# Performance work log

Measured on AMD Instinct MI355X. Metric: run time of the kernel, lower is better.

Reference implementation:

```python
import jax, jax.numpy as jnp
import numpy as np

H, W, D = 56, 56, 28            # input_resolution
WS = (7, 7, 7)                  # window size (Wh, Ww, Wd)
SS = (3, 3, 3)                  # shift size
DIM = 96
NH = 3
HD = DIM // NH
N = WS[0] * WS[1] * WS[2]       # 343 tokens per window
NW = (H // WS[0]) * (W // WS[1]) * (D // WS[2])  # 256 windows


def _rel_pos_index():
    Wd, Wh, Ww = WS
    coords = np.stack(np.meshgrid(np.arange(Wd), np.arange(Wh), np.arange(Ww), indexing='ij'))
    cf = coords.reshape(3, -1)
    rel = (cf[:, :, None] - cf[:, None, :]).transpose(1, 2, 0)
    rel[:, :, 0] += Wd - 1
    rel[:, :, 1] += Wh - 1
    rel[:, :, 2] += Ww - 1
    rel[:, :, 0] *= (2 * Wh - 1) * (2 * Ww - 1)
    rel[:, :, 1] *= (2 * Ww - 1)
    return rel.sum(-1)  # (N, N)


def _attn_mask():
    img = np.zeros((H, W, D), np.float32)
    def slices(w, s):
        return (slice(0, -w), slice(-w, -s), slice(-s, None))
    cnt = 0
    for hs in slices(WS[0], SS[0]):
        for ws in slices(WS[1], SS[1]):
            for ds in slices(WS[2], SS[2]):
                img[hs, ws, ds] = cnt
                cnt += 1
    mw = img.reshape(H // WS[0], WS[0], W // WS[1], WS[1], D // WS[2], WS[2])
    mw = mw.transpose(0, 2, 4, 1, 3, 5).reshape(-1, N)  # (NW, N)
    am = mw[:, None, :] - mw[:, :, None]
    return np.where(am != 0, np.float32(-100.0), np.float32(0.0))


REL_IDX = jnp.asarray(_rel_pos_index())
ATTN_MASK = jnp.asarray(_attn_mask())  # (NW, N, N)


def _ln(x, g, b, eps=1e-5):
    m = x.mean(-1, keepdims=True)
    v = jnp.mean((x - m) ** 2, -1, keepdims=True)
    return (x - m) * jax.lax.rsqrt(v + eps) * g + b


def _forward(x, n1g, n1b, qkv_w, qkv_b, rpb, proj_w, proj_b,
             n2g, n2b, fc1_w, fc1_b, fc2_w, fc2_b):
    B, L, C = x.shape
    shortcut = x
    h = _ln(x, n1g, n1b).reshape(B, H, W, D, C)
    # cyclic shift
    h = jnp.roll(h, (-SS[0], -SS[1], -SS[2]), axis=(1, 2, 3))
    # window partition -> (B*NW, N, C)
    h = h.reshape(B, H // WS[0], WS[0], W // WS[1], WS[1], D // WS[2], WS[2], C)
    h = h.transpose(0, 1, 3, 5, 2, 4, 6, 7).reshape(-1, N, C)
    # qkv
    qkv = (h @ qkv_w + qkv_b).reshape(-1, N, 3, NH, HD).transpose(2, 0, 3, 1, 4)
    q, k, v = qkv[0] * (HD ** -0.5), qkv[1], qkv[2]  # (B*NW, NH, N, HD)
    attn = jnp.einsum('bhnd,bhmd->bhnm', q, k)
    bias = rpb[REL_IDX.reshape(-1)].reshape(N, N, NH).transpose(2, 0, 1)
    attn = attn + bias[None]
    # shifted-window mask
    attn = attn.reshape(B, NW, NH, N, N) + ATTN_MASK[None, :, None]
    attn = jax.nn.softmax(attn.reshape(-1, NH, N, N), axis=-1)
    o = jnp.einsum('bhnm,bhmd->bhnd', attn, v).transpose(0, 2, 1, 3).reshape(-1, N, C)
    o = o @ proj_w + proj_b
    # window reverse
    o = o.reshape(B, H // WS[0], W // WS[1], D // WS[2], WS[0], WS[1], WS[2], C)
    o = o.transpose(0, 1, 4, 2, 5, 3, 6, 7).reshape(B, H, W, D, C)
    o = jnp.roll(o, SS, axis=(1, 2, 3)).reshape(B, L, C)
    x = shortcut + o
    h2 = _ln(x, n2g, n2b)
    h2 = jax.nn.gelu(h2 @ fc1_w + fc1_b, approximate=False) @ fc2_w + fc2_b
    return x + h2


def setup_inputs() -> dict:
    key = jax.random.key(0)
    ks = jax.random.split(key, 6)
    C, FF = DIM, 4 * DIM
    f32 = jnp.float32
    return {
        'x': jax.random.normal(ks[0], (1, H * W * D, C), f32),
        'n1g': jnp.ones((C,), f32), 'n1b': jnp.zeros((C,), f32),
        'qkv_w': jax.random.normal(ks[1], (C, 3 * C), f32) * 0.02,
        'qkv_b': jnp.zeros((3 * C,), f32),
        'rpb': jax.random.normal(ks[2], ((2 * WS[0] - 1) * (2 * WS[1] - 1) * (2 * WS[2] - 1), NH), f32) * 0.02,
        'proj_w': jax.random.normal(ks[3], (C, C), f32) * 0.02,
        'proj_b': jnp.zeros((C,), f32),
        'n2g': jnp.ones((C,), f32), 'n2b': jnp.zeros((C,), f32),
        'fc1_w': jax.random.normal(ks[4], (C, FF), f32) * 0.02,
        'fc1_b': jnp.zeros((FF,), f32),
        'fc2_w': jax.random.normal(ks[5], (FF, C), f32) * 0.02,
        'fc2_b': jnp.zeros((C,), f32),
    }


def reference(x, n1g, n1b, qkv_w, qkv_b, rpb, proj_w, proj_b,
              n2g, n2b, fc1_w, fc1_b, fc2_w, fc2_b):
    return _forward(x, n1g, n1b, qkv_w, qkv_b, rpb, proj_w, proj_b,
                    n2g, n2b, fc1_w, fc1_b, fc2_w, fc2_b)
```

## Files before the change

kernel.cpp:

```cpp
#include <hip/hip_runtime.h>
#include <hip/hip_bf16.h>


#define L_TOK 87808

typedef unsigned int uint;
typedef __attribute__((ext_vector_type(8))) short short8;
typedef __attribute__((ext_vector_type(4))) float f32x4;

__device__ __forceinline__ float bflo(uint u){ union{uint x; float f;} a; a.x = u << 16; return a.f; }
__device__ __forceinline__ float bfhi(uint u){ union{uint x; float f;} a; a.x = u & 0xffff0000u; return a.f; }
__device__ __forceinline__ float bfval(unsigned short w){ union{uint x; float f;} a; a.x = (uint)w << 16; return a.f; }
__device__ __forceinline__ unsigned short f2bfbits(float f){
  union{float f; uint u;} a; a.f = f;
  uint u = a.u;
  u += 0x7fffu + ((u >> 16) & 1u);
  return (unsigned short)(u >> 16);
}
__device__ __forceinline__ unsigned short bfb(float f){
  __hip_bfloat16 h = __float2bfloat16(f);
  return *reinterpret_cast<unsigned short*>(&h);
}
__device__ __forceinline__ uint pkbf(float a, float b){
  return ((uint)bfb(b) << 16) | (uint)bfb(a);
}
__device__ __forceinline__ uint pack2(float a, float b){
  return ((uint)f2bfbits(b) << 16) | (uint)f2bfbits(a);
}
__device__ __forceinline__ uint4 pack8(const float* p){
  uint4 u;
  u.x = pack2(p[0], p[1]); u.y = pack2(p[2], p[3]);
  u.z = pack2(p[4], p[5]); u.w = pack2(p[6], p[7]);
  return u;
}
__device__ __forceinline__ uint4 pack8g(const float* gp){
  float t[8];
  *(float4*)&t[0] = *(const float4*)gp;
  *(float4*)&t[4] = *(const float4*)(gp + 4);
  return pack8(t);
}
__device__ __forceinline__ float gelu_f(float v){
  const float ax = fabsf(v) * 0.70710678118654752f;
  const float t  = 1.0f / (1.0f + 0.3275911f * ax);
  const float poly = t*(0.254829592f + t*(-0.284496736f + t*(1.421413741f +
                     t*(-1.453152027f + t*1.061405429f))));
  float erfv = 1.0f - poly * __expf(-ax*ax);
  erfv = copysignf(erfv, v);
  return 0.5f * v * (1.0f + erfv);
}

__global__ __launch_bounds__(256)
void k_tr(const float* __restrict__ src, unsigned short* __restrict__ dst,
          int K, int N)
{
  const int idx = blockIdx.x * 256 + threadIdx.x;
  if (idx < K * N) {
    const int n = idx / K, k = idx % K;
    dst[idx] = f2bfbits(src[(size_t)k * N + n]);
  }
}

__global__ __launch_bounds__(256)
void k_mb(const float* __restrict__ rpbg, unsigned short* __restrict__ MB)
{
  const int idx = blockIdx.x * 256 + threadIdx.x;
  const int cls = idx / (3*352*352);
  const int rem = idx - cls * (3*352*352);
  const int h = rem / (352*352);
  const int rem2 = rem - h * (352*352);
  const int q = rem2 / 352;
  const int k = rem2 - q * 352;
  unsigned short v = 0xFF80;
  if (q < 343 && k < 343) {
    const int q0 = q/49, q1 = (q%49)/7, q2 = q%7;
    const int k0 = k/49, k1 = (k%49)/7, k2 = k%7;
    const int bq = q0*169 + q1*13 + q2;
    const int bk = k0*169 + k1*13 + k2;
    float bias = rpbg[(size_t)(bq - bk + 1098)*3 + h];
    int cq = 0, ck = 0;
    if (cls & 4) { cq += ((q0 < 4) ? 1 : 2)*9; ck += ((k0 < 4) ? 1 : 2)*9; }
    if (cls & 2) { cq += ((q1 < 4) ? 1 : 2)*3; ck += ((k1 < 4) ? 1 : 2)*3; }
    if (cls & 1) { cq += (q2 < 4) ? 1 : 2;     ck += (k2 < 4) ? 1 : 2; }
    if (cq != ck) bias -= 100.0f;
    v = f2bfbits(bias);
  }
  MB[idx] = v;
}

__global__ __launch_bounds__(256)
void k_qkv_ln(const float* __restrict__ x,
              const float* __restrict__ n1g,
              const float* __restrict__ n1b,
              const unsigned short* __restrict__ qkvwt,
              const float* __restrict__ bias, size_t headStride,
              __hip_bfloat16* __restrict__ qb,
              __hip_bfloat16* __restrict__ kb,
              __hip_bfloat16* __restrict__ vb)
{
  __shared__ __align__(16) unsigned short As[64][104];
  __shared__ uint srcOff[64];
  __shared__ float gLds[96], bLds[96];
  __shared__ float pSum[256], pSq[256];
  __shared__ float mLds[64], sLds[64];

  const int tid = threadIdx.x;
  const int wave = tid >> 6, lane = tid & 63;
  const int row0 = blockIdx.x * 64;

  if (tid < 64) {
    const uint row = (uint)(row0 + tid);
    const uint win = row / 343u, n = row % 343u;
    const uint wh = win >> 5, ww = (win >> 2) & 7u, wd = win & 3u;
    const uint ih = n / 49u, rr = n % 49u, iw = rr / 7u, id = rr % 7u;
    uint gh = wh*7u + ih + 3u; if (gh >= 56u) gh -= 56u;
    uint gw = ww*7u + iw + 3u; if (gw >= 56u) gw -= 56u;
    uint gd = wd*7u + id + 3u; if (gd >= 28u) gd -= 28u;
    srcOff[tid] = ((gh*56u + gw)*28u + gd) * 96u;
  }
  if (tid < 96) { gLds[tid] = n1g[tid]; bLds[tid] = n1b[tid]; }
  __syncthreads();

  for (int i = tid; i < 768; i += 256) {
    const int r = i / 12, kk = (i % 12) * 8;
    *(uint4*)&As[r][kk] = pack8g(x + srcOff[r] + kk);
  }
  __syncthreads();

  {
    const int r = tid & 63, seg = tid >> 6;
    float s = 0.0f, sq = 0.0f;
    #pragma unroll
    for (int j3 = 0; j3 < 3; ++j3) {
      const uint4 u = *(const uint4*)&As[r][seg*24 + j3*8];
      float v[8];
      v[0]=bflo(u.x); v[1]=bfhi(u.x); v[2]=bflo(u.y); v[3]=bfhi(u.y);
      v[4]=bflo(u.z); v[5]=bfhi(u.z); v[6]=bflo(u.w); v[7]=bfhi(u.w);
      #pragma unroll
      for (int j = 0; j < 8; ++j) { s += v[j]; sq += v[j]*v[j]; }
    }
    pSum[tid] = s; pSq[tid] = sq;
  }
  __syncthreads();
  if (tid < 64) {
    const float s  = pSum[tid] + pSum[tid+64] + pSum[tid+128] + pSum[tid+192];
    const float sq = pSq[tid] + pSq[tid+64] + pSq[tid+128] + pSq[tid+192];
    const float mean = s * (1.0f/96.0f);
    mLds[tid] = mean;
    sLds[tid] = rsqrtf(sq*(1.0f/96.0f) - mean*mean + 1e-5f);
  }
  __syncthreads();
  for (int i = tid; i < 768; i += 256) {
    const int r = i / 12, kk = (i % 12) * 8;
    uint4 u = *(uint4*)&As[r][kk];
    const float m = mLds[r], sc = sLds[r];
    float v[8];
    v[0]=bflo(u.x); v[1]=bfhi(u.x); v[2]=bflo(u.y); v[3]=bfhi(u.y);
    v[4]=bflo(u.z); v[5]=bfhi(u.z); v[6]=bflo(u.w); v[7]=bfhi(u.w);
    #pragma unroll
    for (int j = 0; j < 8; ++j) v[j] = (v[j] - m)*sc*gLds[kk+j] + bLds[kk+j];
    *(uint4*)&As[r][kk] = pack8(v);
  }
  __syncthreads();

  f32x4 acc[18];
  #pragma unroll
  for (int i = 0; i < 18; ++i) acc[i] = (f32x4){0.f, 0.f, 0.f, 0.f};
  const int ml = lane & 15, q8 = (lane >> 4) * 8;
  #pragma unroll
  for (int kc = 0; kc < 3; ++kc) {
    const short8 a = *(const short8*)&As[wave*16 + ml][kc*32 + q8];
    #pragma unroll
    for (int nt = 0; nt < 18; ++nt) {
      const short8 b = *(const short8*)(qkvwt + (size_t)(nt*16 + ml)*96 + kc*32 + q8);
      acc[nt] = __builtin_amdgcn_mfma_f32_16x16x32_bf16(a, b, acc[nt], 0, 0, 0);
    }
  }

  const float qscale = 0.17677669529663687f;
  #pragma unroll
  for (int nt = 0; nt < 18; ++nt) {
    const int nbase = nt * 16;
    const int part = nbase / 96;
    const int rem  = nbase - part * 96;
    const int h    = rem >> 5;
    const int dbase= rem & 31;
    __hip_bfloat16* base = (part == 0) ? qb : ((part == 1) ? kb : vb);
    __hip_bfloat16* dst = base + (size_t)h * headStride;
    const float bv = bias[nbase + ml];
    #pragma unroll
    for (int r = 0; r < 4; ++r) {
      const size_t row = (size_t)(row0 + wave*16 + (lane >> 4)*4 + r);
      float v = acc[nt][r] + bv;
      if (part == 0) v *= qscale;
      dst[row*32 + dbase + ml] = __float2bfloat16(v);
    }
  }
}

__global__ __launch_bounds__(256, 4)
void k_attn_v10(const __hip_bfloat16* __restrict__ qg,
                const __hip_bfloat16* __restrict__ kg,
                const __hip_bfloat16* __restrict__ vg,
                size_t headStride,
                const unsigned short* __restrict__ MB,
                float* __restrict__ ob)
{
  __shared__ __align__(16) unsigned short vt[32*344 + 16];
  __shared__ __align__(16) unsigned short Pc[4][16*56];
  __shared__ float lred[4][16];

  const int tid = threadIdx.x;
  const int wave = tid >> 6, lane = tid & 63;
  const uint win = blockIdx.x;
  const int hh = (int)blockIdx.y;
  const int mtBase = (int)blockIdx.z * 11;
  const size_t wbase = (size_t)hh * headStride + (size_t)win * (343*32);
  const unsigned short* qw = (const unsigned short*)qg + wbase;
  const unsigned short* kw = (const unsigned short*)kg + wbase;
  const unsigned short* vw = (const unsigned short*)vg + wbase;

  const uint wh = win >> 5, ww = (win >> 2) & 7u, wd = win & 3u;
  const int cls = ((wh == 7u) ? 4 : 0) | ((ww == 7u) ? 2 : 0) | ((wd == 3u) ? 1 : 0);
  const unsigned short* MBh = MB + ((size_t)cls*3 + hh) * (352*352);

  for (int t = tid; t < 343; t += 256) {
    const uint4* src = (const uint4*)(vw + (size_t)t*32);
    #pragma unroll
    for (int c4 = 0; c4 < 4; ++c4) {
      const uint4 u = src[c4];
      const int d = c4*8;
      vt[(d+0)*344 + t] = (unsigned short)(u.x & 0xffffu);
      vt[(d+1)*344 + t] = (unsigned short)(u.x >> 16);
      vt[(d+2)*344 + t] = (unsigned short)(u.y & 0xffffu);
      vt[(d+3)*344 + t] = (unsigned short)(u.y >> 16);
      vt[(d+4)*344 + t] = (unsigned short)(u.z & 0xffffu);
      vt[(d+5)*344 + t] = (unsigned short)(u.z >> 16);
      vt[(d+6)*344 + t] = (unsigned short)(u.w & 0xffffu);
      vt[(d+7)*344 + t] = (unsigned short)(u.w >> 16);
    }
  }
  if (tid < 32) vt[tid*344 + 343] = 0;
  if (tid < 16) vt[32*344 + tid] = 0;
  __syncthreads();

  const int ml = lane & 15, g = lane >> 4, g8 = g*8;
  unsigned short* Pw = &Pc[wave][0];

  for (int mt = mtBase + wave; mt < mtBase + 11; mt += 4) {
    const int q = mt*16 + ml;
    const short8 qf = *(const short8*)(qw + (size_t)q*32 + g8);
    const unsigned short* MBq = MBh + (size_t)q * 352;
    float l = 0.0f;
    f32x4 o0 = {0.f,0.f,0.f,0.f}, o1 = {0.f,0.f,0.f,0.f};

    for (int kc = 0; kc < 11; ++kc) {
      const short8 kf0 = *(const short8*)(kw + (size_t)(kc*32 + ml)*32 + g8);
      const short8 kf1 = *(const short8*)(kw + (size_t)(kc*32 + 16 + ml)*32 + g8);
      f32x4 s0 = __builtin_amdgcn_mfma_f32_16x16x32_bf16(kf0, qf, (f32x4){0.f,0.f,0.f,0.f}, 0, 0, 0);
      f32x4 s1 = __builtin_amdgcn_mfma_f32_16x16x32_bf16(kf1, qf, (f32x4){0.f,0.f,0.f,0.f}, 0, 0, 0);

      const ushort4 u0 = *(const ushort4*)(MBq + kc*32 + 4*g);
      const ushort4 u1 = *(const ushort4*)(MBq + kc*32 + 16 + 4*g);

      float p0 = __expf(s0[0] + bfval(u0.x));
      float p1 = __expf(s0[1] + bfval(u0.y));
      float p2 = __expf(s0[2] + bfval(u0.z));
      float p3 = __expf(s0[3] + bfval(u0.w));
      float p4 = __expf(s1[0] + bfval(u1.x));
      float p5 = __expf(s1[1] + bfval(u1.y));
      float p6 = __expf(s1[2] + bfval(u1.z));
      float p7 = __expf(s1[3] + bfval(u1.w));
      l += ((p0 + p1) + (p2 + p3)) + ((p4 + p5) + (p6 + p7));

      uint2 wlo, whi;
      wlo.x = pkbf(p0, p1); wlo.y = pkbf(p2, p3);
      whi.x = pkbf(p4, p5); whi.y = pkbf(p6, p7);
      *(uint2*)&Pw[ml*56 + 4*g]      = wlo;
      *(uint2*)&Pw[ml*56 + 16 + 4*g] = whi;

      const short8 pf  = *(const short8*)&Pw[ml*56 + g8];
      const short8 vf0 = *(const short8*)&vt[(size_t)ml*344 + kc*32 + g8];
      const short8 vf1 = *(const short8*)&vt[(size_t)(16 + ml)*344 + kc*32 + g8];
      o0 = __builtin_amdgcn_mfma_f32_16x16x32_bf16(pf, vf0, o0, 0, 0, 0);
      o1 = __builtin_amdgcn_mfma_f32_16x16x32_bf16(pf, vf1, o1, 0, 0, 0);
    }

    l += __shfl_xor(l, 16);
    l += __shfl_xor(l, 32);
    if (g == 0) lred[wave][ml] = 1.0f / l;
    const float4 li = *(const float4*)&lred[wave][4*g];
    #pragma unroll
    for (int r = 0; r < 4; ++r) {
      const int row = mt*16 + 4*g + r;
      if (row < 343) {
        float* op = ob + ((size_t)win*343 + (uint)row)*96 + hh*32;
        op[ml]      = o0[r] * li[r];
        op[16 + ml] = o1[r] * li[r];
      }
    }
  }
}

__global__ __launch_bounds__(256, 4)
void k_attn_v9(const __hip_bfloat16* __restrict__ qg,
               const __hip_bfloat16* __restrict__ kg,
               const __hip_bfloat16* __restrict__ vg,
               size_t headStride,
               const float* __restrict__ rpbg,
               float* __restrict__ ob)
{
  __shared__ __align__(16) unsigned short vt[32*344 + 16];
  __shared__ __align__(16) unsigned short Pc[4][16*40];
  __shared__ short baseT[352];
  __shared__ unsigned char cntT[352];
  __shared__ unsigned short rpB[2197];

  const int tid = threadIdx.x;
  const int wave = tid >> 6, lane = tid & 63;
  const uint win = blockIdx.x;
  const int hh = (int)blockIdx.y;
  const int mtBase = (int)blockIdx.z * 11;
  const size_t wbase = (size_t)hh * headStride + (size_t)win * (343*32);
  const unsigned short* qw = (const unsigned short*)qg + wbase;
  const unsigned short* kw = (const unsigned short*)kg + wbase;
  const unsigned short* vw = (const unsigned short*)vg + wbase;

  for (int i = tid; i < 2197; i += 256) rpB[i] = f2bfbits(rpbg[i*3 + hh]);
  const uint wh = win >> 5, ww = (win >> 2) & 7u, wd = win & 3u;
  for (int i = tid; i < 352; i += 256) {
    if (i < 343) {
      const uint c0 = (uint)i/49u, rr = (uint)i%49u, c1 = rr/7u, c2 = rr%7u;
      baseT[i] = (short)(c0*169u + c1*13u + c2);
      const uint g0 = wh*7u + c0, g1 = ww*7u + c1, g2 = wd*7u + c2;
      const uint rh = (g0 < 49u) ? 0u : ((g0 < 53u) ? 1u : 2u);
      const uint rw = (g1 < 49u) ? 0u : ((g1 < 53u) ? 1u : 2u);
      const uint rd = (g2 < 21u) ? 0u : ((g2 < 25u) ? 1u : 2u);
      cntT[i] = (unsigned char)(rh*9u + rw*3u + rd);
    } else { baseT[i] = 0; cntT[i] = 255; }
  }
  for (int t = tid; t < 343; t += 256) {
    const uint4* src = (const uint4*)(vw + (size_t)t*32);
    #pragma unroll
    for (int c4 = 0; c4 < 4; ++c4) {
      const uint4 u = src[c4];
      const int d = c4*8;
      vt[(d+0)*344 + t] = (unsigned short)(u.x & 0xffffu);
      vt[(d+1)*344 + t] = (unsigned short)(u.x >> 16);
      vt[(d+2)*344 + t] = (unsigned short)(u.y & 0xffffu);
      vt[(d+3)*344 + t] = (unsigned short)(u.y >> 16);
      vt[(d+4)*344 + t] = (unsigned short)(u.z & 0xffffu);
      vt[(d+5)*344 + t] = (unsigned short)(u.z >> 16);
      vt[(d+6)*344 + t] = (unsigned short)(u.w & 0xffffu);
      vt[(d+7)*344 + t] = (unsigned short)(u.w >> 16);
    }
  }
  if (tid < 32) vt[tid*344 + 343] = 0;
  if (tid < 16) vt[32*344 + tid] = 0;
  __syncthreads();

  const int ml = lane & 15, g = lane >> 4, g8 = g*8;
  unsigned short* Pw = &Pc[wave][0];

  for (int mt = mtBase + wave; mt < mtBase + 11; mt += 4) {
    const int qrow = mt*16;
    const short8 qf = *(const short8*)(qw + (size_t)(qrow + ml)*32 + g8);
    int cnR[4], biR[4];
    #pragma unroll
    for (int r = 0; r < 4; ++r) {
      const int gi = qrow + g*4 + r;
      cnR[r] = (int)cntT[gi];
      biR[r] = (int)baseT[gi] + 1098;
    }
    float m_[4], l_[4];
    #pragma unroll
    for (int r = 0; r < 4; ++r) { m_[r] = -1e30f; l_[r] = 0.0f; }
    f32x4 o0 = {0.f,0.f,0.f,0.f}, o1 = {0.f,0.f,0.f,0.f};

    for (int kc = 0; kc < 11; ++kc) {
      const int c0 = kc*32 + ml, c1 = c0 + 16;
      const short8 kf0 = *(const short8*)(kw + (size_t)c0*32 + g8);
      const short8 kf1 = *(const short8*)(kw + (size_t)c1*32 + g8);
      f32x4 s0 = __builtin_amdgcn_mfma_f32_16x16x32_bf16(qf, kf0, (f32x4){0.f,0.f,0.f,0.f}, 0, 0, 0);
      f32x4 s1 = __builtin_amdgcn_mfma_f32_16x16x32_bf16(qf, kf1, (f32x4){0.f,0.f,0.f,0.f}, 0, 0, 0);

      float bv0[4], bv1[4];
      const int bj0 = (int)baseT[c0], bj1 = (int)baseT[c1];
      #pragma unroll
      for (int r = 0; r < 4; ++r) {
        bv0[r] = bfval(rpB[biR[r] - bj0]);
        bv1[r] = bfval(rpB[biR[r] - bj1]);
      }
      const int cj0 = (int)cntT[c0], cj1 = (int)cntT[c1];

      float a_[4];
      #pragma unroll
      for (int r = 0; r < 4; ++r) {
        float v0 = s0[r] + bv0[r];
        float v1 = s1[r] + bv1[r];
        v0 += (cj0 == cnR[r]) ? 0.0f : -100.0f;
        v1 += (cj1 == cnR[r]) ? 0.0f : -100.0f;
        v1 = (c1 < 343) ? v1 : -1e30f;
        s0[r] = v0; s1[r] = v1;
        float cm = fmaxf(v0, v1);
        cm = fmaxf(cm, __shfl_xor(cm, 1));
        cm = fmaxf(cm, __shfl_xor(cm, 2));
        cm = fmaxf(cm, __shfl_xor(cm, 4));
        cm = fmaxf(cm, __shfl_xor(cm, 8));
        const float mn = fmaxf(m_[r], cm);
        a_[r] = __expf(m_[r] - mn);
        m_[r] = mn;
      }
      #pragma unroll
      for (int r = 0; r < 4; ++r) {
        const float p0 = __expf(s0[r] - m_[r]);
        const float p1 = __expf(s1[r] - m_[r]);
        Pw[(g*4 + r)*40 + ml]      = f2bfbits(p0);
        Pw[(g*4 + r)*40 + 16 + ml] = f2bfbits(p1);
        float cs = p0 + p1;
        cs += __shfl_xor(cs, 1);
        cs += __shfl_xor(cs, 2);
        cs += __shfl_xor(cs, 4);
        cs += __shfl_xor(cs, 8);
        l_[r] = l_[r]*a_[r] + cs;
        o0[r] *= a_[r];
        o1[r] *= a_[r];
      }
      const short8 pf  = *(const short8*)&Pw[ml*40 + g8];
      const short8 vf0 = *(const short8*)&vt[(size_t)ml*344 + kc*32 + g8];
      const short8 vf1 = *(const short8*)&vt[(size_t)(16 + ml)*344 + kc*32 + g8];
      o0 = __builtin_amdgcn_mfma_f32_16x16x32_bf16(pf, vf0, o0, 0, 0, 0);
      o1 = __builtin_amdgcn_mfma_f32_16x16x32_bf16(pf, vf1, o1, 0, 0, 0);
    }

    #pragma unroll
    for (int r = 0; r < 4; ++r) {
      const int row = qrow + g*4 + r;
      if (row < 343) {
        const float inv = 1.0f / l_[r];
        float* op = ob + ((size_t)win*343 + (uint)row)*96 + hh*32;
        op[ml]      = o0[r] * inv;
        op[16 + ml] = o1[r] * inv;
      }
    }
  }
}

__global__ __launch_bounds__(256)
void k_proj(const float* __restrict__ A,
            const unsigned short* __restrict__ pwt,
            const float* __restrict__ bias,
            const float* __restrict__ xin,
            __hip_bfloat16* __restrict__ xres)
{
  __shared__ __align__(16) unsigned short As[128][104];
  const int tid = threadIdx.x;
  const int wave = tid >> 6, lane = tid & 63;
  const int row0 = blockIdx.x * 128;

  for (int i = tid; i < 1536; i += 256) {
    const int r = i / 12, kk = (i % 12) * 8;
    *(uint4*)&As[r][kk] = pack8g(A + (size_t)(row0 + r)*96 + kk);
  }
  __syncthreads();

  f32x4 acc[2][6];
  #pragma unroll
  for (int mt = 0; mt < 2; ++mt)
    #pragma unroll
    for (int i = 0; i < 6; ++i) acc[mt][i] = (f32x4){0.f, 0.f, 0.f, 0.f};
  const int ml = lane & 15, q8 = (lane >> 4) * 8;
  #pragma unroll
  for (int kc = 0; kc < 3; ++kc) {
    const short8 a0 = *(const short8*)&As[wave*32 + ml][kc*32 + q8];
    const short8 a1 = *(const short8*)&As[wave*32 + 16 + ml][kc*32 + q8];
    #pragma unroll
    for (int nt = 0; nt < 6; ++nt) {
      const short8 b = *(const short8*)(pwt + (size_t)(nt*16 + ml)*96 + kc*32 + q8);
      acc[0][nt] = __builtin_amdgcn_mfma_f32_16x16x32_bf16(a0, b, acc[0][nt], 0, 0, 0);
      acc[1][nt] = __builtin_amdgcn_mfma_f32_16x16x32_bf16(a1, b, acc[1][nt], 0, 0, 0);
    }
  }

  #pragma unroll
  for (int mt = 0; mt < 2; ++mt) {
    #pragma unroll
    for (int r = 0; r < 4; ++r) {
      const uint row = (uint)(row0 + wave*32 + mt*16 + (lane >> 4)*4 + r);
      const uint win = row / 343u, n = row % 343u;
      const uint wh = win >> 5, ww = (win >> 2) & 7u, wd = win & 3u;
      const uint ih = n / 49u, rr = n % 49u, iw = rr / 7u, id = rr % 7u;
      uint gh = wh*7u + ih + 3u; if (gh >= 56u) gh -= 56u;
      uint gw = ww*7u + iw + 3u; if (gw >= 56u) gw -= 56u;
      uint gd = wd*7u + id + 3u; if (gd >= 28u) gd -= 28u;
      const size_t gt = (size_t)((gh*56u + gw)*28u + gd) * 96;
      #pragma unroll
      for (int nt = 0; nt < 6; ++nt) {
        const int col = nt*16 + ml;
        xres[gt + col] = __float2bfloat16(acc[mt][nt][r] + bias[col] + xin[gt + col]);
      }
    }
  }
}

__global__ __launch_bounds__(256, 4)
void k_mlp(const __hip_bfloat16* __restrict__ xresb,
           const float* __restrict__ n2g,
           const float* __restrict__ n2b,
           const unsigned short* __restrict__ w1t,
           const float* __restrict__ b1,
           const unsigned short* __restrict__ w2t,
           const float* __restrict__ b2,
           float* __restrict__ out)
{
  __shared__ __align__(16) unsigned short As[64][104];
  __shared__ __align__(16) unsigned short inter[64][200];
  float* scr  = (float*)&inter[0][0];
  float* pSum = scr;
  float* pSq  = scr + 256;
  float* gL   = scr + 512;
  float* bL   = scr + 608;
  float* mL   = scr + 704;
  float* sL   = scr + 768;

  const int tid = threadIdx.x;
  const int wave = tid >> 6, lane = tid & 63;
  const int row0 = blockIdx.x * 64;
  const int ml = lane & 15, g = lane >> 4, g8 = g*8;

  if (tid < 96) { gL[tid] = n2g[tid]; bL[tid] = n2b[tid]; }
  for (int i = tid; i < 768; i += 256) {
    const int r = i / 12, kk = (i % 12) * 8;
    *(uint4*)&As[r][kk] = *(const uint4*)(xresb + (size_t)(row0 + r)*96 + kk);
  }
  __syncthreads();

  {
    const int r = tid & 63, seg = tid >> 6;
    float s = 0.0f, sq = 0.0f;
    #pragma unroll
    for (int j3 = 0; j3 < 3; ++j3) {
      const uint4 u = *(const uint4*)&As[r][seg*24 + j3*8];
      float v[8];
      v[0]=bflo(u.x); v[1]=bfhi(u.x); v[2]=bflo(u.y); v[3]=bfhi(u.y);
      v[4]=bflo(u.z); v[5]=bfhi(u.z); v[6]=bflo(u.w); v[7]=bfhi(u.w);
      #pragma unroll
      for (int j = 0; j < 8; ++j) { s += v[j]; sq += v[j]*v[j]; }
    }
    pSum[tid] = s; pSq[tid] = sq;
  }
  __syncthreads();
  if (tid < 64) {
    const float s  = pSum[tid] + pSum[tid+64] + pSum[tid+128] + pSum[tid+192];
    const float sq = pSq[tid] + pSq[tid+64] + pSq[tid+128] + pSq[tid+192];
    const float mean = s * (1.0f/96.0f);
    mL[tid] = mean;
    sL[tid] = rsqrtf(sq*(1.0f/96.0f) - mean*mean + 1e-5f);
  }
  __syncthreads();
  for (int i = tid; i < 768; i += 256) {
    const int r = i / 12, kk = (i % 12) * 8;
    uint4 u = *(uint4*)&As[r][kk];
    const float m = mL[r], sc = sL[r];
    float v[8];
    v[0]=bflo(u.x); v[1]=bfhi(u.x); v[2]=bflo(u.y); v[3]=bfhi(u.y);
    v[4]=bflo(u.z); v[5]=bfhi(u.z); v[6]=bflo(u.w); v[7]=bfhi(u.w);
    #pragma unroll
    for (int j = 0; j < 8; ++j) v[j] = (v[j] - m)*sc*gL[kk+j] + bL[kk+j];
    *(uint4*)&As[r][kk] = pack8(v);
  }
  __syncthreads();

  short8 af[4][3];
  #pragma unroll
  for (int mt = 0; mt < 4; ++mt)
    #pragma unroll
    for (int kc = 0; kc < 3; ++kc)
      af[mt][kc] = *(const short8*)&As[mt*16 + ml][kc*32 + g8];

  const int rb = 32 * (wave >> 1);
  const int cb = 48 * (wave & 1);
  f32x4 acc2[2][3];
  #pragma unroll
  for (int i = 0; i < 2; ++i)
    #pragma unroll
    for (int nt = 0; nt < 3; ++nt)
      acc2[i][nt] = (f32x4){0.f, 0.f, 0.f, 0.f};

  #pragma unroll
  for (int H = 0; H < 2; ++H) {
    if (H) __syncthreads();

    const int nbg = H*192 + 48*wave;
    const int cl0 = 48*wave;
    short8 bf[3][3];
    #pragma unroll
    for (int nt = 0; nt < 3; ++nt)
      #pragma unroll
      for (int kc = 0; kc < 3; ++kc)
        bf[nt][kc] = *(const short8*)(w1t + (size_t)(nbg + 16*nt + ml)*96 + kc*32 + g8);

    f32x4 acc[4][3];
    #pragma unroll
    for (int mt = 0; mt < 4; ++mt)
      #pragma unroll
      for (int nt = 0; nt < 3; ++nt)
        acc[mt][nt] = (f32x4){0.f, 0.f, 0.f, 0.f};

    #pragma unroll
    for (int kc = 0; kc < 3; ++kc)
      #pragma unroll
      for (int nt = 0; nt < 3; ++nt)
        #pragma unroll
        for (int mt = 0; mt < 4; ++mt)
          acc[mt][nt] = __builtin_amdgcn_mfma_f32_16x16x32_bf16(af[mt][kc], bf[nt][kc], acc[mt][nt], 0, 0, 0);

    #pragma unroll
    for (int nt = 0; nt < 3; ++nt) {
      const float b1v = b1[nbg + 16*nt + ml];
      const int c = cl0 + 16*nt + ml;
      #pragma unroll
      for (int mt = 0; mt < 4; ++mt) {
        #pragma unroll
        for (int r = 0; r < 4; ++r) {
          inter[mt*16 + 4*g + r][c] = f2bfbits(gelu_f(acc[mt][nt][r] + b1v));
        }
      }
    }
    __syncthreads();

    #pragma unroll
    for (int kcl = 0; kcl < 6; ++kcl) {
      const short8 a0 = *(const short8*)&inter[rb + ml][kcl*32 + g8];
      const short8 a1 = *(const short8*)&inter[rb + 16 + ml][kcl*32 + g8];
      #pragma unroll
      for (int nt = 0; nt < 3; ++nt) {
        const short8 b = *(const short8*)(w2t + (size_t)(cb + 16*nt + ml)*384 + H*192 + kcl*32 + g8);
        acc2[0][nt] = __builtin_amdgcn_mfma_f32_16x16x32_bf16(a0, b, acc2[0][nt], 0, 0, 0);
        acc2[1][nt] = __builtin_amdgcn_mfma_f32_16x16x32_bf16(a1, b, acc2[1][nt], 0, 0, 0);
      }
    }
  }

  const unsigned short* xu = (const unsigned short*)xresb;
  #pragma unroll
  for (int i = 0; i < 2; ++i) {
    #pragma unroll
    for (int nt = 0; nt < 3; ++nt) {
      const int col = cb + 16*nt + ml;
      const float b2v = b2[col];
      #pragma unroll
      for (int r = 0; r < 4; ++r) {
        const size_t row = (size_t)(row0 + rb + 16*i + 4*g + r);
        out[row*96 + col] = acc2[i][nt][r] + b2v + bfval(xu[row*96 + col]);
      }
    }
  }
}

extern "C" void kernel_launch(void* const* d_in, const int* in_sizes, int n_in,
                              void* d_out, int out_size, void* d_ws, size_t ws_size,
                              hipStream_t stream)
{
  (void)in_sizes; (void)n_in; (void)out_size;
  const float* x    = (const float*)d_in[0];
  const float* n1g  = (const float*)d_in[1];
  const float* n1b  = (const float*)d_in[2];
  const float* qkvw = (const float*)d_in[3];
  const float* qkvb = (const float*)d_in[4];
  const float* rpb  = (const float*)d_in[5];
  const float* pw   = (const float*)d_in[6];
  const float* pb   = (const float*)d_in[7];
  const float* n2g  = (const float*)d_in[8];
  const float* n2b  = (const float*)d_in[9];
  const float* f1w  = (const float*)d_in[10];
  const float* f1b  = (const float*)d_in[11];
  const float* f2w  = (const float*)d_in[12];
  const float* f2b  = (const float*)d_in[13];
  float* out = (float*)d_out;

  const size_t E = (size_t)L_TOK * 96;
  __hip_bfloat16* qb = (__hip_bfloat16*)d_ws;
  __hip_bfloat16* kb = qb + E;
  __hip_bfloat16* vb = kb + E;
  __hip_bfloat16* xres = (__hip_bfloat16*)d_ws;
  float* ob = out;
  const size_t hs = (size_t)L_TOK * 32;

  unsigned short* qkvwt = (unsigned short*)d_out;
  unsigned short* pwt   = (unsigned short*)kb;
  unsigned short* w1t   = pwt + 9216;
  unsigned short* w2t   = w1t + 36864;

  const size_t MB_BYTES = (size_t)8 * 3 * 352 * 352 * 2;
  unsigned short* MBp = nullptr;
  if (ws_size >= (size_t)6 * E + MB_BYTES) {
    MBp = (unsigned short*)((char*)d_ws + (size_t)6 * E);
    k_mb<<<11616, 256, 0, stream>>>(rpb, MBp);
  }

  k_tr<<<108, 256, 0, stream>>>(qkvw, qkvwt, 96, 288);
  k_qkv_ln<<<L_TOK/64, 256, 0, stream>>>(
      x, n1g, n1b, qkvwt, qkvb, hs, qb, kb, vb);
  if (MBp)
    k_attn_v10<<<dim3(256, 3, 2), 256, 0, stream>>>(qb, kb, vb, hs, MBp, ob);
  else
    k_attn_v9<<<dim3(256, 3, 2), 256, 0, stream>>>(qb, kb, vb, hs, rpb, ob);
  k_tr<<<36, 256, 0, stream>>>(pw, pwt, 96, 96);
  k_tr<<<144, 256, 0, stream>>>(f1w, w1t, 96, 384);
  k_tr<<<144, 256, 0, stream>>>(f2w, w2t, 384, 96);
  k_proj<<<L_TOK/128, 256, 0, stream>>>(ob, pwt, pb, x, xres);
  k_mlp<<<L_TOK/64, 256, 0, stream>>>(xres, n2g, n2b, w1t, f1b, w2t, f2b, out);
}
```

Baseline: 294.6 us.

## Fuse projection, residual, LayerNorm2 and MLP into one kernel with bf16 attention output

Attention now writes its output as bf16 into a separate workspace buffer instead of fp32. A new kernel k_pm does the output projection, first residual add, second LayerNorm, fc1+GELU and fc2+residual in one pass per 64-row tile. The residual stays in shared memory rather than round-tripping through global memory. This removes one launch and the global traffic for the fp32 attention output and the bf16 residual. In exchange it needs more workspace, drops the v9 fallback (the non-fused path may now call v10 with a null bias table), and uses heavier per-block shared memory, so occupancy is lower.

```diff
diff --git a/kernel.cpp b/kernel.cpp
--- a/kernel.cpp
+++ b/kernel.cpp
@@ -47,6 +47,15 @@
   float erfv = 1.0f - poly * __expf(-ax*ax);
   erfv = copysignf(erfv, v);
   return 0.5f * v * (1.0f + erfv);
+}
+__device__ __forceinline__ uint gt_of_row(uint row){
+  const uint win = row / 343u, n = row % 343u;
+  const uint wh = win >> 5, ww = (win >> 2) & 7u, wd = win & 3u;
+  const uint ih = n / 49u, rr = n % 49u, iw = rr / 7u, id = rr % 7u;
+  uint gh = wh*7u + ih + 3u; if (gh >= 56u) gh -= 56u;
+  uint gw = ww*7u + iw + 3u; if (gw >= 56u) gw -= 56u;
+  uint gd = wd*7u + id + 3u; if (gd >= 28u) gd -= 28u;
+  return ((gh*56u + gw)*28u + gd) * 96u;
 }
 
 __global__ __launch_bounds__(256)
@@ -107,16 +116,7 @@
   const int wave = tid >> 6, lane = tid & 63;
   const int row0 = blockIdx.x * 64;
 
-  if (tid < 64) {
-    const uint row = (uint)(row0 + tid);
-    const uint win = row / 343u, n = row % 343u;
-    const uint wh = win >> 5, ww = (win >> 2) & 7u, wd = win & 3u;
-    const uint ih = n / 49u, rr = n % 49u, iw = rr / 7u, id = rr % 7u;
-    uint gh = wh*7u + ih + 3u; if (gh >= 56u) gh -= 56u;
-    uint gw = ww*7u + iw + 3u; if (gw >= 56u) gw -= 56u;
-    uint gd = wd*7u + id + 3u; if (gd >= 28u) gd -= 28u;
-    srcOff[tid] = ((gh*56u + gw)*28u + gd) * 96u;
-  }
+  if (tid < 64) srcOff[tid] = gt_of_row((uint)(row0 + tid));
   if (tid < 96) { gLds[tid] = n1g[tid]; bLds[tid] = n1b[tid]; }
   __syncthreads();
 
@@ -197,13 +197,14 @@
   }
 }
 
+template<bool BF16OUT>
 __global__ __launch_bounds__(256, 4)
 void k_attn_v10(const __hip_bfloat16* __restrict__ qg,
                 const __hip_bfloat16* __restrict__ kg,
                 const __hip_bfloat16* __restrict__ vg,
                 size_t headStride,
                 const unsigned short* __restrict__ MB,
-                float* __restrict__ ob)
+                void* __restrict__ obp)
 {
   __shared__ __align__(16) unsigned short vt[32*344 + 16];
   __shared__ __align__(16) unsigned short Pc[4][16*56];
@@ -293,153 +294,205 @@
     for (int r = 0; r < 4; ++r) {
       const int row = mt*16 + 4*g + r;
       if (row < 343) {
-        float* op = ob + ((size_t)win*343 + (uint)row)*96 + hh*32;
-        op[ml]      = o0[r] * li[r];
-        op[16 + ml] = o1[r] * li[r];
-      }
-    }
-  }
-}
-
-__global__ __launch_bounds__(256, 4)
-void k_attn_v9(const __hip_bfloat16* __restrict__ qg,
-               const __hip_bfloat16* __restrict__ kg,
-               const __hip_bfloat16* __restrict__ vg,
-               size_t headStride,
-               const float* __restrict__ rpbg,
-               float* __restrict__ ob)
+        const size_t base = ((size_t)win*343 + (uint)row)*96 + hh*32;
+        if (BF16OUT) {
+          __hip_bfloat16* op = (__hip_bfloat16*)obp + base;
+          op[ml]      = __float2bfloat16(o0[r] * li[r]);
+          op[16 + ml] = __float2bfloat16(o1[r] * li[r]);
+        } else {
+          float* op = (float*)obp + base;
+          op[ml]      = o0[r] * li[r];
+          op[16 + ml] = o1[r] * li[r];
+        }
+      }
+    }
+  }
+}
+
+__global__ __launch_bounds__(256, 2)
+void k_pm(const __hip_bfloat16* __restrict__ obb,
+          const unsigned short* __restrict__ pwt,
+          const float* __restrict__ pb,
+          const float* __restrict__ xin,
+          const float* __restrict__ n2g,
+          const float* __restrict__ n2b,
+          const unsigned short* __restrict__ w1t,
+          const float* __restrict__ b1,
+          const unsigned short* __restrict__ w2t,
+          const float* __restrict__ b2,
+          float* __restrict__ out)
 {
-  __shared__ __align__(16) unsigned short vt[32*344 + 16];
-  __shared__ __align__(16) unsigned short Pc[4][16*40];
-  __shared__ short baseT[352];
-  __shared__ unsigned char cntT[352];
-  __shared__ unsigned short rpB[2197];
+  __shared__ __align__(16) unsigned short As[64][104];
+  __shared__ __align__(16) unsigned short Rs[64][104];
+  __shared__ __align__(16) unsigned short inter[64][200];
+  __shared__ uint gtO[64];
+  float* scr  = (float*)&inter[0][0];
+  float* pSum = scr;
+  float* pSq  = scr + 256;
+  float* gL   = scr + 512;
+  float* bL   = scr + 608;
+  float* mL   = scr + 704;
+  float* sL   = scr + 768;
 
   const int tid = threadIdx.x;
   const int wave = tid >> 6, lane = tid & 63;
-  const uint win = blockIdx.x;
-  const int hh = (int)blockIdx.y;
-  const int mtBase = (int)blockIdx.z * 11;
-  const size_t wbase = (size_t)hh * headStride + (size_t)win * (343*32);
-  const unsigned short* qw = (const unsigned short*)qg + wbase;
-  const unsigned short* kw = (const unsigned short*)kg + wbase;
-  const unsigned short* vw = (const unsigned short*)vg + wbase;
-
-  for (int i = tid; i < 2197; i += 256) rpB[i] = f2bfbits(rpbg[i*3 + hh]);
-  const uint wh = win >> 5, ww = (win >> 2) & 7u, wd = win & 3u;
-  for (int i = tid; i < 352; i += 256) {
-    if (i < 343) {
-      const uint c0 = (uint)i/49u, rr = (uint)i%49u, c1 = rr/7u, c2 = rr%7u;
-      baseT[i] = (short)(c0*169u + c1*13u + c2);
-      const uint g0 = wh*7u + c0, g1 = ww*7u + c1, g2 = wd*7u + c2;
-      const uint rh = (g0 < 49u) ? 0u : ((g0 < 53u) ? 1u : 2u);
-      const uint rw = (g1 < 49u) ? 0u : ((g1 < 53u) ? 1u : 2u);
-      const uint rd = (g2 < 21u) ? 0u : ((g2 < 25u) ? 1u : 2u);
-      cntT[i] = (unsigned char)(rh*9u + rw*3u + rd);
-    } else { baseT[i] = 0; cntT[i] = 255; }
-  }
-  for (int t = tid; t < 343; t += 256) {
-    const uint4* src = (const uint4*)(vw + (size_t)t*32);
-    #pragma unroll
-    for (int c4 = 0; c4 < 4; ++c4) {
-      const uint4 u = src[c4];
-      const int d = c4*8;
-      vt[(d+0)*344 + t] = (unsigned short)(u.x & 0xffffu);
-      vt[(d+1)*344 + t] = (unsigned short)(u.x >> 16);
-      vt[(d+2)*344 + t] = (unsigned short)(u.y & 0xffffu);
-      vt[(d+3)*344 + t] = (unsigned short)(u.y >> 16);
-      vt[(d+4)*344 + t] = (unsigned short)(u.z & 0xffffu);
-      vt[(d+5)*344 + t] = (unsigned short)(u.z >> 16);
-      vt[(d+6)*344 + t] = (unsigned short)(u.w & 0xffffu);
-      vt[(d+7)*344 + t] = (unsigned short)(u.w >> 16);
-    }
-  }
-  if (tid < 32) vt[tid*344 + 343] = 0;
-  if (tid < 16) vt[32*344 + tid] = 0;
-  __syncthreads();
-
+  const int row0 = blockIdx.x * 64;
   const int ml = lane & 15, g = lane >> 4, g8 = g*8;
-  unsigned short* Pw = &Pc[wave][0];
-
-  for (int mt = mtBase + wave; mt < mtBase + 11; mt += 4) {
-    const int qrow = mt*16;
-    const short8 qf = *(const short8*)(qw + (size_t)(qrow + ml)*32 + g8);
-    int cnR[4], biR[4];
-    #pragma unroll
-    for (int r = 0; r < 4; ++r) {
-      const int gi = qrow + g*4 + r;
-      cnR[r] = (int)cntT[gi];
-      biR[r] = (int)baseT[gi] + 1098;
-    }
-    float m_[4], l_[4];
-    #pragma unroll
-    for (int r = 0; r < 4; ++r) { m_[r] = -1e30f; l_[r] = 0.0f; }
-    f32x4 o0 = {0.f,0.f,0.f,0.f}, o1 = {0.f,0.f,0.f,0.f};
-
-    for (int kc = 0; kc < 11; ++kc) {
-      const int c0 = kc*32 + ml, c1 = c0 + 16;
-      const short8 kf0 = *(const short8*)(kw + (size_t)c0*32 + g8);
-      const short8 kf1 = *(const short8*)(kw + (size_t)c1*32 + g8);
-      f32x4 s0 = __builtin_amdgcn_mfma_f32_16x16x32_bf16(qf, kf0, (f32x4){0.f,0.f,0.f,0.f}, 0, 0, 0);
-      f32x4 s1 = __builtin_amdgcn_mfma_f32_16x16x32_bf16(qf, kf1, (f32x4){0.f,0.f,0.f,0.f}, 0, 0, 0);
-
-      float bv0[4], bv1[4];
-      const int bj0 = (int)baseT[c0], bj1 = (int)baseT[c1];
+
+  if (tid < 64) gtO[tid] = gt_of_row((uint)(row0 + tid));
+  if (tid < 96) { gL[tid] = n2g[tid]; bL[tid] = n2b[tid]; }
+  for (int i = tid; i < 768; i += 256) {
+    const int r = i / 12, kk = (i % 12) * 8;
+    *(uint4*)&As[r][kk] = *(const uint4*)(obb + (size_t)(row0 + r)*96 + kk);
+  }
+  __syncthreads();
+
+  {
+    short8 paf[3];
+    #pragma unroll
+    for (int kc = 0; kc < 3; ++kc)
+      paf[kc] = *(const short8*)&As[wave*16 + ml][kc*32 + g8];
+    f32x4 acc[6];
+    #pragma unroll
+    for (int i = 0; i < 6; ++i) acc[i] = (f32x4){0.f, 0.f, 0.f, 0.f};
+    #pragma unroll
+    for (int kc = 0; kc < 3; ++kc)
+      #pragma unroll
+      for (int nt = 0; nt < 6; ++nt) {
+        const short8 b = *(const short8*)(pwt + (size_t)(nt*16 + ml)*96 + kc*32 + g8);
+        acc[nt] = __builtin_amdgcn_mfma_f32_16x16x32_bf16(paf[kc], b, acc[nt], 0, 0, 0);
+      }
+    #pragma unroll
+    for (int nt = 0; nt < 6; ++nt) {
+      const int col = nt*16 + ml;
+      const float pbv = pb[col];
       #pragma unroll
       for (int r = 0; r < 4; ++r) {
-        bv0[r] = bfval(rpB[biR[r] - bj0]);
-        bv1[r] = bfval(rpB[biR[r] - bj1]);
-      }
-      const int cj0 = (int)cntT[c0], cj1 = (int)cntT[c1];
-
-      float a_[4];
+        const int rl = wave*16 + 4*g + r;
+        const float v = acc[nt][r] + pbv + xin[(size_t)gtO[rl] + col];
+        Rs[rl][col] = f2bfbits(v);
+      }
+    }
+  }
+  __syncthreads();
+
+  {
+    const int r = tid & 63, seg = tid >> 6;
+    float s = 0.0f, sq = 0.0f;
+    #pragma unroll
+    for (int j3 = 0; j3 < 3; ++j3) {
+      const uint4 u = *(const uint4*)&Rs[r][seg*24 + j3*8];
+      float v[8];
+      v[0]=bflo(u.x); v[1]=bfhi(u.x); v[2]=bflo(u.y); v[3]=bfhi(u.y);
+      v[4]=bflo(u.z); v[5]=bfhi(u.z); v[6]=bflo(u.w); v[7]=bfhi(u.w);
+      #pragma unroll
+      for (int j = 0; j < 8; ++j) { s += v[j]; sq += v[j]*v[j]; }
+    }
+    pSum[tid] = s; pSq[tid] = sq;
+  }
+  __syncthreads();
+  if (tid < 64) {
+    const float s  = pSum[tid] + pSum[tid+64] + pSum[tid+128] + pSum[tid+192];
+    const float sq = pSq[tid] + pSq[tid+64] + pSq[tid+128] + pSq[tid+192];
+    const float mean = s * (1.0f/96.0f);
+    mL[tid] = mean;
+    sL[tid] = rsqrtf(sq*(1.0f/96.0f) - mean*mean + 1e-5f);
+  }
+  __syncthreads();
+  for (int i = tid; i < 768; i += 256) {
+    const int r = i / 12, kk = (i % 12) * 8;
+    uint4 u = *(uint4*)&Rs[r][kk];
+    const float m = mL[r], sc = sL[r];
+    float v[8];
+    v[0]=bflo(u.x); v[1]=bfhi(u.x); v[2]=bflo(u.y); v[3]=bfhi(u.y);
+    v[4]=bflo(u.z); v[5]=bfhi(u.z); v[6]=bflo(u.w); v[7]=bfhi(u.w);
+    #pragma unroll
+    for (int j = 0; j < 8; ++j) v[j] = (v[j] - m)*sc*gL[kk+j] + bL[kk+j];
+    *(uint4*)&As[r][kk] = pack8(v);
+  }
+  __syncthreads();
+
+  short8 af[4][3];
+  #pragma unroll
+  for (int mt = 0; mt < 4; ++mt)
+    #pragma unroll
+    for (int kc = 0; kc < 3; ++kc)
+      af[mt][kc] = *(const short8*)&As[mt*16 + ml][kc*32 + g8];
+
+  const int rb = 32 * (wave >> 1);
+  const int cb = 48 * (wave & 1);
+  f32x4 acc2[2][3];
+  #pragma unroll
+  for (int i = 0; i < 2; ++i)
+    #pragma unroll
+    for (int nt = 0; nt < 3; ++nt)
+      acc2[i][nt] = (f32x4){0.f, 0.f, 0.f, 0.f};
+
+  #pragma unroll
+  for (int H = 0; H < 2; ++H) {
+    if (H) __syncthreads();
+
+    const int nbg = H*192 + 48*wave;
+    const int cl0 = 48*wave;
+    short8 bf[3][3];
+    #pragma unroll
+    for (int nt = 0; nt < 3; ++nt)
+      #pragma unroll
+      for (int kc = 0; kc < 3; ++kc)
+        bf[nt][kc] = *(const short8*)(w1t + (size_t)(nbg + 16*nt + ml)*96 + kc*32 + g8);
+
+    f32x4 acc[4][3];
+    #pragma unroll
+    for (int mt = 0; mt < 4; ++mt)
+      #pragma unroll
+      for (int nt = 0; nt < 3; ++nt)
+        acc[mt][nt] = (f32x4){0.f, 0.f, 0.f, 0.f};
+
+    #pragma unroll
+    for (int kc = 0; kc < 3; ++kc)
+      #pragma unroll
+      for (int nt = 0; nt < 3; ++nt)
+        #pragma unroll
+        for (int mt = 0; mt < 4; ++mt)
+          acc[mt][nt] = __builtin_amdgcn_mfma_f32_16x16x32_bf16(af[mt][kc], bf[nt][kc], acc[mt][nt], 0, 0, 0);
+
+    #pragma unroll
+    for (int nt = 0; nt < 3; ++nt) {
+      const float b1v = b1[nbg + 16*nt + ml];
+      const int c = cl0 + 16*nt + ml;
+      #pragma unroll
+      for (int mt = 0; mt < 4; ++mt) {
+        #pragma unroll
+        for (int r = 0; r < 4; ++r) {
+          inter[mt*16 + 4*g + r][c] = f2bfbits(gelu_f(acc[mt][nt][r] + b1v));
+        }
+      }
+    }
+    __syncthreads();
+
+    #pragma unroll
+    for (int kcl = 0; kcl < 6; ++kcl) {
+      const short8 a0 = *(const short8*)&inter[rb + ml][kcl*32 + g8];
+      const short8 a1 = *(const short8*)&inter[rb + 16 + ml][kcl*32 + g8];
+      #pragma unroll
+      for (int nt = 0; nt < 3; ++nt) {
+        const short8 b = *(const short8*)(w2t + (size_t)(cb + 16*nt + ml)*384 + H*192 + kcl*32 + g8);
+        acc2[0][nt] = __builtin_amdgcn_mfma_f32_16x16x32_bf16(a0, b, acc2[0][nt], 0, 0, 0);
+        acc2[1][nt] = __builtin_amdgcn_mfma_f32_16x16x32_bf16(a1, b, acc2[1][nt], 0, 0, 0);
+      }
+    }
+  }
+
+  #pragma unroll
+  for (int i = 0; i < 2; ++i) {
+    #pragma unroll
+    for (int nt = 0; nt < 3; ++nt) {
+      const int col = cb + 16*nt + ml;
+      const float b2v = b2[col];
       #pragma unroll
       for (int r = 0; r < 4; ++r) {
-        float v0 = s0[r] + bv0[r];
-        float v1 = s1[r] + bv1[r];
-        v0 += (cj0 == cnR[r]) ? 0.0f : -100.0f;
-        v1 += (cj1 == cnR[r]) ? 0.0f : -100.0f;
-        v1 = (c1 < 343) ? v1 : -1e30f;
-        s0[r] = v0; s1[r] = v1;
-        float cm = fmaxf(v0, v1);
-        cm = fmaxf(cm, __shfl_xor(cm, 1));
-        cm = fmaxf(cm, __shfl_xor(cm, 2));
-        cm = fmaxf(cm, __shfl_xor(cm, 4));
-        cm = fmaxf(cm, __shfl_xor(cm, 8));
-        const float mn = fmaxf(m_[r], cm);
-        a_[r] = __expf(m_[r] - mn);
-        m_[r] = mn;
-      }
-      #pragma unroll
-      for (int r = 0; r < 4; ++r) {
-        const float p0 = __expf(s0[r] - m_[r]);
-        const float p1 = __expf(s1[r] - m_[r]);
-        Pw[(g*4 + r)*40 + ml]      = f2bfbits(p0);
-        Pw[(g*4 + r)*40 + 16 + ml] = f2bfbits(p1);
-        float cs = p0 + p1;
-        cs += __shfl_xor(cs, 1);
-        cs += __shfl_xor(cs, 2);
-        cs += __shfl_xor(cs, 4);
-        cs += __shfl_xor(cs, 8);
-        l_[r] = l_[r]*a_[r] + cs;
-        o0[r] *= a_[r];
-        o1[r] *= a_[r];
-      }
-      const short8 pf  = *(const short8*)&Pw[ml*40 + g8];
-      const short8 vf0 = *(const short8*)&vt[(size_t)ml*344 + kc*32 + g8];
-      const short8 vf1 = *(const short8*)&vt[(size_t)(16 + ml)*344 + kc*32 + g8];
-      o0 = __builtin_amdgcn_mfma_f32_16x16x32_bf16(pf, vf0, o0, 0, 0, 0);
-      o1 = __builtin_amdgcn_mfma_f32_16x16x32_bf16(pf, vf1, o1, 0, 0, 0);
-    }
-
-    #pragma unroll
-    for (int r = 0; r < 4; ++r) {
-      const int row = qrow + g*4 + r;
-      if (row < 343) {
-        const float inv = 1.0f / l_[r];
-        float* op = ob + ((size_t)win*343 + (uint)row)*96 + hh*32;
-        op[ml]      = o0[r] * inv;
-        op[16 + ml] = o1[r] * inv;
+        const int rl = rb + 16*i + 4*g + r;
+        out[(size_t)gtO[rl] + col] = acc2[i][nt][r] + b2v + bfval(Rs[rl][col]);
       }
     }
   }
@@ -486,13 +539,7 @@
     #pragma unroll
     for (int r = 0; r < 4; ++r) {
       const uint row = (uint)(row0 + wave*32 + mt*16 + (lane >> 4)*4 + r);
-      const uint win = row / 343u, n = row % 343u;
-      const uint wh = win >> 5, ww = (win >> 2) & 7u, wd = win & 3u;
-      const uint ih = n / 49u, rr = n % 49u, iw = rr / 7u, id = rr % 7u;
-      uint gh = wh*7u + ih + 3u; if (gh >= 56u) gh -= 56u;
-      uint gw = ww*7u + iw + 3u; if (gw >= 56u) gw -= 56u;
-      uint gd = wd*7u + id + 3u; if (gd >= 28u) gd -= 28u;
-      const size_t gt = (size_t)((gh*56u + gw)*28u + gd) * 96;
+      const size_t gt = (size_t)gt_of_row(row);
       #pragma unroll
       for (int nt = 0; nt < 6; ++nt) {
         const int col = nt*16 + ml;
@@ -683,7 +730,6 @@
   __hip_bfloat16* kb = qb + E;
   __hip_bfloat16* vb = kb + E;
   __hip_bfloat16* xres = (__hip_bfloat16*)d_ws;
-  float* ob = out;
   const size_t hs = (size_t)L_TOK * 32;
 
   unsigned short* qkvwt = (unsigned short*)d_out;
@@ -692,22 +738,31 @@
   unsigned short* w2t   = w1t + 36864;
 
   const size_t MB_BYTES = (size_t)8 * 3 * 352 * 352 * 2;
-  unsigned short* MBp = nullptr;
-  if (ws_size >= (size_t)6 * E + MB_BYTES) {
-    MBp = (unsigned short*)((char*)d_ws + (size_t)6 * E);
-    k_mb<<<11616, 256, 0, stream>>>(rpb, MBp);
-  }
+  const bool mbok  = ws_size >= (size_t)6 * E + MB_BYTES;
+  const bool fused = ws_size >= (size_t)8 * E + MB_BYTES;
+  unsigned short* MBp = mbok ? (unsigned short*)((char*)d_ws + (size_t)6 * E) : nullptr;
+  __hip_bfloat16* obb = fused ? (__hip_bfloat16*)((char*)d_ws + (size_t)6 * E + MB_BYTES) : nullptr;
+
+  if (MBp) k_mb<<<11616, 256, 0, stream>>>(rpb, MBp);
 
   k_tr<<<108, 256, 0, stream>>>(qkvw, qkvwt, 96, 288);
   k_qkv_ln<<<L_TOK/64, 256, 0, stream>>>(
       x, n1g, n1b, qkvwt, qkvb, hs, qb, kb, vb);
-  if (MBp)
-    k_attn_v10<<<dim3(256, 3, 2), 256, 0, stream>>>(qb, kb, vb, hs, MBp, ob);
-  else
-    k_attn_v9<<<dim3(256, 3, 2), 256, 0, stream>>>(qb, kb, vb, hs, rpb, ob);
-  k_tr<<<36, 256, 0, stream>>>(pw, pwt, 96, 96);
-  k_tr<<<144, 256, 0, stream>>>(f1w, w1t, 96, 384);
-  k_tr<<<144, 256, 0, stream>>>(f2w, w2t, 384, 96);
-  k_proj<<<L_TOK/128, 256, 0, stream>>>(ob, pwt, pb, x, xres);
-  k_mlp<<<L_TOK/64, 256, 0, stream>>>(xres, n2g, n2b, w1t, f1b, w2t, f2b, out);
-}
+
+  if (fused && MBp) {
+    k_attn_v10<true><<<dim3(256, 3, 2), 256, 0, stream>>>(qb, kb, vb, hs, MBp, (void*)obb);
+    k_tr<<<36, 256, 0, stream>>>(pw, pwt, 96, 96);
+    k_tr<<<144, 256, 0, stream>>>(f1w, w1t, 96, 384);
+    k_tr<<<144, 256, 0, stream>>>(f2w, w2t, 384, 96);
+    k_pm<<<L_TOK/64, 256, 0, stream>>>(obb, pwt, pb, x, n2g, n2b,
+                                       w1t, f1b, w2t, f2b, out);
+  } else {
+    float* ob = out;
+    k_attn_v10<false><<<dim3(256, 3, 2), 256, 0, stream>>>(qb, kb, vb, hs, MBp, (void*)ob);
+    k_tr<<<36, 256, 0, stream>>>(pw, pwt, 96, 96);
+    k_tr<<<144, 256, 0, stream>>>(f1w, w1t, 96, 384);
+    k_tr<<<144, 256, 0, stream>>>(f2w, w2t, 384, 96);
+    k_proj<<<L_TOK/128, 256, 0, stream>>>(ob, pwt, pb, x, xres);
+    k_mlp<<<L_TOK/64, 256, 0, stream>>>(xres, n2g, n2b, w1t, f1b, w2t, f2b, out);
+  }
+}
```

After: 276.8 us. 6.0% less time.
